# Performance work log

Hardware: AMD Instinct MI355X
Metric: run time of the kernel (lower is better)

Reference implementation:

```python
import jax, jax.numpy as jnp
import numpy as np

NX = 65536   # spatial cells
T = 32       # time points
H = 128      # MLP hidden width
DX = 1.0     # spatial resolution (init kwarg dx)
S0, S1 = -1.0, 1.0  # fixed stencil (learn_stencil=False)


def setup_inputs() -> dict:
    key = jax.random.key(0)
    k1, k2, k3, k4 = jax.random.split(key, 4)
    t = jnp.arange(T, dtype=jnp.float32) * 0.01          # time grid, dt=0.01
    u0 = jax.random.uniform(k1, (NX,), jnp.float32)      # initial state
    inv_sqrt_h = jnp.float32(1.0 / np.sqrt(H))
    W1 = jax.random.normal(k2, (1, H), jnp.float32)
    W2 = jax.random.normal(k3, (H, H), jnp.float32) * inv_sqrt_h
    W3 = jax.random.normal(k4, (H, 1), jnp.float32) * inv_sqrt_h
    D = jnp.full((1,), 0.01, jnp.float32)                # diffusion coefficient
    BC = jnp.zeros((2, 1), jnp.float32)                  # Dirichlet BC values
    return {"t": t, "u0": u0, "W1": W1, "W2": W2, "W3": W3, "D": D, "BC": BC}


def _flux(u, W1, W2, W3, D, BC):
    # per-cell MLP (func_nn): Linear->Tanh->Linear->Tanh->Linear, no bias, no sigmoid
    h = jnp.tanh(u[:, None] @ W1)        # [Nx, H]
    h = jnp.tanh(h @ W2)                 # [Nx, H]
    a = (h @ W3)[:, 0]                   # [Nx]
    a_plus = jax.nn.relu(a)
    a_min = -jax.nn.relu(-a)
    d = D[0]
    # left fluxes
    lb = d * (S0 * u[0] + S1 * BC[0, 0]) - a_plus[0] / DX * (-S0 * u[0] - S1 * BC[0, 0])
    ln = d * (S0 * u[1:] + S1 * u[:-1]) - a_plus[1:] / DX * (-S0 * u[1:] - S1 * u[:-1])
    left = jnp.concatenate([lb[None], ln])
    # right fluxes
    rb = d * (S0 * u[-1] + S1 * BC[1, 0]) - a_min[-1] / DX * (S0 * u[-1] + S1 * BC[1, 0])
    rn = d * (S0 * u[:-1] + S1 * u[1:]) - a_min[:-1] / DX * (S0 * u[:-1] + S1 * u[1:])
    right = jnp.concatenate([rn, rb[None]])
    return left + right


def reference(t, u0, W1, W2, W3, D, BC):
    # Neural-ODE integration of du/dt = flux_kernel(u); fixed-step RK4 over grid t
    f = lambda u: _flux(u, W1, W2, W3, D, BC)

    def step(u, dt):
        k1 = f(u)
        k2 = f(u + 0.5 * dt * k1)
        k3 = f(u + 0.5 * dt * k2)
        k4 = f(u + dt * k3)
        un = u + (dt / 6.0) * (k1 + 2.0 * k2 + 2.0 * k3 + k4)
        return un, un

    _, us = jax.lax.scan(step, u0, jnp.diff(t))
    return jnp.concatenate([u0[None], us], axis=0)  # [T, Nx]
```

## Files before the change

### kernel.cpp

```cpp
#include <hip/hip_runtime.h>

#define NXC 65536
#define TT 32
#define HH 128
#define TABN 6145
#define TABNP 6146
#define TABLO (-1.0f)
#define TABINV 2048.0f
#define OUTW 64
#define VC 3
#define WINW 192
#define HALO 64

typedef __attribute__((ext_vector_type(8))) short bf16x8;
typedef __attribute__((ext_vector_type(4))) float f32x4;
typedef unsigned short u16;

__device__ __forceinline__ float bf2f(u16 b) {
    union { unsigned int u; float f; } v; v.u = ((unsigned int)b) << 16; return v.f;
}
__device__ __forceinline__ u16 f2bf(float f) {
    union { float f; unsigned int u; } v; v.f = f;
    return (u16)((v.u + 0x7fffu + ((v.u >> 16) & 1u)) >> 16);
}
__device__ __forceinline__ bool is_bf16_mode(const void* t) {
    return ((const u16*)t)[1] != 0;
}

#if __has_builtin(__builtin_amdgcn_exp2f)
#define EXP2F(x) __builtin_amdgcn_exp2f(x)
#else
#define EXP2F(x) exp2f(x)
#endif
#if __has_builtin(__builtin_amdgcn_rcpf)
#define RCPF(x) __builtin_amdgcn_rcpf(x)
#else
#define RCPF(x) (1.0f / (x))
#endif
#if __has_builtin(__builtin_amdgcn_fractf)
#define FRACTF(x) __builtin_amdgcn_fractf(x)
#else
#define FRACTF(x) ((x) - floorf(x))
#endif

__device__ __forceinline__ float fast_tanh(float x) {
    float e = EXP2F(x * 2.8853900817779268f);
    return 1.0f - 2.0f * RCPF(e + 1.0f);
}

__device__ __forceinline__ float dpp_up1(float x) {
    int xi = __float_as_int(x);
    int r = __builtin_amdgcn_update_dpp(xi, xi, 0x138, 0xf, 0xf, false);
    return __int_as_float(r);
}
__device__ __forceinline__ float dpp_dn1(float x) {
    int xi = __float_as_int(x);
    int r = __builtin_amdgcn_update_dpp(xi, xi, 0x130, 0xf, 0xf, false);
    return __int_as_float(r);
}

__global__ void w2swz_kernel(const void* t, const void* W2,
                             u16* __restrict__ w2frag) {
    bool bf = is_bf16_mode(t);
    int i = blockIdx.x * 256 + threadIdx.x;
    int j = i & 7;
    int lane = (i >> 3) & 63;
    int ks = (i >> 9) & 3;
    int nt = i >> 11;
    int k = ks * 32 + (lane >> 4) * 8 + j;
    int n = nt * 16 + (lane & 15);
    w2frag[i] = bf ? ((const u16*)W2)[k * HH + n]
                   : f2bf(((const float*)W2)[k * HH + n]);
}

__global__ __launch_bounds__(256) void tabbuild_kernel(
    const void* traw, const void* W1, const void* W3,
    const u16* __restrict__ w2frag, float* __restrict__ atab) {
    __shared__ float w1s[HH];
    __shared__ float w3s[HH];
    bool bf = is_bf16_mode(traw);
    int tid = threadIdx.x;
    if (tid < HH)
        w1s[tid] = bf ? bf2f(((const u16*)W1)[tid]) : ((const float*)W1)[tid];
    else
        w3s[tid - HH] = bf ? bf2f(((const u16*)W3)[tid - HH])
                           : ((const float*)W3)[tid - HH];
    __syncthreads();

    int lane = tid & 63;
    int wave = tid >> 6;
    int q = lane >> 4;
    int m = lane & 15;
    int base = (blockIdx.x * 4 + wave) * 16;
    float uin = TABLO + (float)(base + m) * (1.0f / TABINV);

    bf16x8 afrag[4];
#pragma unroll
    for (int ks = 0; ks < 4; ++ks)
#pragma unroll
        for (int j = 0; j < 8; ++j) {
            float h = fast_tanh(uin * w1s[ks * 32 + q * 8 + j]);
            afrag[ks][j] = (short)f2bf(h);
        }

    const bf16x8* w2f = (const bf16x8*)w2frag;
    float p0 = 0.f, p1 = 0.f, p2 = 0.f, p3 = 0.f;
#pragma unroll
    for (int nt = 0; nt < 8; ++nt) {
        f32x4 acc = {0.f, 0.f, 0.f, 0.f};
#pragma unroll
        for (int ks = 0; ks < 4; ++ks) {
            bf16x8 b = w2f[(nt * 4 + ks) * 64 + lane];
            acc = __builtin_amdgcn_mfma_f32_16x16x32_bf16(afrag[ks], b, acc, 0, 0, 0);
        }
        float w3v = w3s[nt * 16 + m];
        p0 += fast_tanh(acc[0]) * w3v;
        p1 += fast_tanh(acc[1]) * w3v;
        p2 += fast_tanh(acc[2]) * w3v;
        p3 += fast_tanh(acc[3]) * w3v;
    }
#pragma unroll
    for (int sh = 1; sh < 16; sh <<= 1) {
        p0 += __shfl_xor(p0, sh, 64);
        p1 += __shfl_xor(p1, sh, 64);
        p2 += __shfl_xor(p2, sh, 64);
        p3 += __shfl_xor(p3, sh, 64);
    }
    int r = m & 3;
    float a = (r == 0) ? p0 : (r == 1) ? p1 : (r == 2) ? p2 : p3;
    if (m < 4) {
        int e = base + q * 4 + r;
        if (e < TABNP) atab[e] = a;
    }
}

__global__ __launch_bounds__(256) void chunk_kernel(
    const void* traw, const void* uin, float* __restrict__ uout,
    const void* Draw, const void* BCraw, const float* __restrict__ atab,
    void* __restrict__ outbase, int s0, int nsteps) {
    __shared__ __align__(16) float2 tab[TABN];
    __shared__ float t32s[TT];

    int tid = threadIdx.x;
    bool bf = is_bf16_mode(traw);

    for (int e = tid * 4; e < TABN - 1; e += 1024) {
        float4 qv = *(const float4*)(atab + e);
        float nx = atab[e + 4];
        float4 lo = make_float4(qv.x, qv.y - qv.x, qv.y, qv.z - qv.y);
        float4 hi = make_float4(qv.z, qv.w - qv.z, qv.w, nx - qv.w);
        *(float4*)(&tab[e]) = lo;
        *(float4*)(&tab[e + 2]) = hi;
    }
    if (tid == 0)
        tab[TABN - 1] = make_float2(atab[TABN - 1], atab[TABN] - atab[TABN - 1]);
    if (tid < TT)
        t32s[tid] = bf ? bf2f(((const u16*)traw)[tid]) : ((const float*)traw)[tid];

    float d   = bf ? bf2f(((const u16*)Draw)[0])  : ((const float*)Draw)[0];
    float bc0 = bf ? bf2f(((const u16*)BCraw)[0]) : ((const float*)BCraw)[0];
    float bc1 = bf ? bf2f(((const u16*)BCraw)[1]) : ((const float*)BCraw)[1];

    int lane = tid & 63;
    int wid = blockIdx.x * 4 + (tid >> 6);
    int gb = wid * OUTW - HALO + lane * VC;
    int i0 = lane * VC;
    bool first = (s0 == 0);
    bool edgeblk = (blockIdx.x == 0) || (blockIdx.x == gridDim.x - 1);

    float v[VC], ub[VC], gfix[VC];
    bool gok[VC], own[VC];
#pragma unroll
    for (int j = 0; j < VC; ++j) {
        int g = gb + j;
        int i = i0 + j;
        gok[j] = (g >= 0) && (g < NXC);
        own[j] = (i >= HALO) && (i < HALO + OUTW);
        float x;
        if (first) {
            if (bf) {
                u16 raw = gok[j] ? ((const u16*)uin)[g] : (u16)0;
                x = bf2f(raw);
                if (own[j]) ((u16*)outbase)[g] = raw;
            } else {
                float raw = gok[j] ? ((const float*)uin)[g] : 0.f;
                x = raw;
                if (own[j]) ((float*)outbase)[g] = raw;
            }
        } else {
            x = gok[j] ? ((const float*)uin)[g] : 0.f;
        }
        if (!gok[j]) x = (g < 0) ? bc0 : bc1;
        gfix[j] = x;
        v[j] = x;
        ub[j] = x;
    }
    __syncthreads();

    float pf[VC];
    float2 pt[VC];
#pragma unroll
    for (int j = 0; j < VC; ++j) {
        float f = fmaf(v[j], TABINV, (-TABLO) * TABINV);
        f = fminf(fmaxf(f, 0.0f), (float)(TABN - 1));
        int e0 = (int)f;
        pf[j] = FRACTF(f);
        pt[j] = tab[e0];
    }

    for (int st = 0; st < nsteps; ++st) {
        int step = s0 + st;
        float dt = t32s[step + 1] - t32s[step];
        float dt2 = 0.5f * dt, dt6 = dt * (1.0f / 6.0f);
        float kacc[VC], kv[VC];
#pragma unroll
        for (int j = 0; j < VC; ++j) kacc[j] = 0.f;
#pragma unroll
        for (int s = 0; s < 4; ++s) {
            float cnext = (s < 2) ? dt2 : dt;
            float wgt = (s == 1 || s == 2) ? 2.f : 1.f;
            float vup = dpp_up1(v[VC - 1]);
            float vdn = dpp_dn1(v[0]);
#pragma unroll
            for (int j = 0; j < VC; ++j) {
                float vc = v[j];
                float vl = (j == 0) ? vup : v[j - 1];
                float vr = (j == VC - 1) ? vdn : v[j + 1];
                float a = fmaf(pf[j], pt[j].y, pt[j].x);
                float ap = fmaxf(a, 0.f);
                float am = fminf(a, 0.f);
                kv[j] = (vl - vc) * (d + ap) + (vr - vc) * (d - am);
            }
#pragma unroll
            for (int j = 0; j < VC; ++j) {
                kacc[j] += wgt * kv[j];
                float nv = (s < 3) ? fmaf(cnext, kv[j], ub[j])
                                   : fmaf(dt6, kacc[j], ub[j]);
                v[j] = nv;
                if (s == 3) ub[j] = nv;
                float f = fmaf(v[j], TABINV, (-TABLO) * TABINV);
                f = fminf(fmaxf(f, 0.0f), (float)(TABN - 1));
                int e0 = (int)f;
                pf[j] = FRACTF(f);
                pt[j] = tab[e0];
            }
            if (edgeblk) {
#pragma unroll
                for (int j = 0; j < VC; ++j)
                    if (!gok[j]) { v[j] = gfix[j]; ub[j] = gfix[j]; }
            }
        }
        if (bf) {
            u16* orow = (u16*)outbase + (size_t)(step + 1) * NXC;
#pragma unroll
            for (int j = 0; j < VC; ++j)
                if (own[j]) orow[gb + j] = f2bf(ub[j]);
        } else {
            float* orow = (float*)outbase + (size_t)(step + 1) * NXC;
#pragma unroll
            for (int j = 0; j < VC; ++j)
                if (own[j]) orow[gb + j] = ub[j];
        }
    }
    if (uout != nullptr) {
#pragma unroll
        for (int j = 0; j < VC; ++j)
            if (own[j]) uout[gb + j] = ub[j];
    }
}

extern "C" void kernel_launch(void* const* d_in, const int* in_sizes, int n_in,
                              void* d_out, int out_size, void* d_ws,
                              size_t ws_size, hipStream_t stream) {
    const void* t  = d_in[0];
    const void* u0 = d_in[1];
    const void* W1 = d_in[2];
    const void* W2 = d_in[3];
    const void* W3 = d_in[4];
    const void* Dp = d_in[5];
    const void* BC = d_in[6];

    float* atab = (float*)d_ws;
    u16* w2frag = (u16*)(atab + TABNP + 2);
    float* uB = (float*)(w2frag + 16384);

    w2swz_kernel<<<64, 256, 0, stream>>>(t, W2, w2frag);
    tabbuild_kernel<<<(TABNP + 63) / 64, 256, 0, stream>>>(t, W1, W3, w2frag, atab);

    chunk_kernel<<<NXC / (OUTW * 4), 256, 0, stream>>>(t, u0, uB, Dp, BC, atab,
                                                       d_out, 0, 16);
    chunk_kernel<<<NXC / (OUTW * 4), 256, 0, stream>>>(t, uB, nullptr, Dp, BC, atab,
                                                       d_out, 16, 15);
}
```

Measured before the change: 98.23 us.

## Process two interleaved 32-cell windows per wave with a wider halo

Each wave now integrates two independent 192-cell windows. Each window owns 32 output cells and carries an 80-cell halo, where before a single window owned 64 outputs with a 64-cell halo. The launch grid stays the same size, so each thread holds twice the state. The two independent dependency chains are meant to give instruction-level parallelism that hides the LDS table-lookup and DPP latency at the low wave occupancy of one block per CU. The cost is twice as much redundant halo computation per output cell, plus more registers.

```diff
diff --git a/kernel.cpp b/kernel.cpp
--- a/kernel.cpp
+++ b/kernel.cpp
@@ -7,10 +7,11 @@
 #define TABNP 6146
 #define TABLO (-1.0f)
 #define TABINV 2048.0f
-#define OUTW 64
+#define OUTW 32
 #define VC 3
 #define WINW 192
-#define HALO 64
+#define HALO 80
+#define NW 2
 
 typedef __attribute__((ext_vector_type(8))) short bf16x8;
 typedef __attribute__((ext_vector_type(4))) float f32x4;
@@ -163,109 +164,136 @@
 
     int lane = tid & 63;
     int wid = blockIdx.x * 4 + (tid >> 6);
-    int gb = wid * OUTW - HALO + lane * VC;
     int i0 = lane * VC;
     bool first = (s0 == 0);
     bool edgeblk = (blockIdx.x == 0) || (blockIdx.x == gridDim.x - 1);
 
-    float v[VC], ub[VC], gfix[VC];
-    bool gok[VC], own[VC];
+    int gbw[NW];
+    float v[NW][VC], ub[NW][VC], gfix[NW][VC];
+    bool gok[NW][VC], own[VC];
 #pragma unroll
     for (int j = 0; j < VC; ++j) {
-        int g = gb + j;
         int i = i0 + j;
-        gok[j] = (g >= 0) && (g < NXC);
         own[j] = (i >= HALO) && (i < HALO + OUTW);
-        float x;
-        if (first) {
-            if (bf) {
-                u16 raw = gok[j] ? ((const u16*)uin)[g] : (u16)0;
-                x = bf2f(raw);
-                if (own[j]) ((u16*)outbase)[g] = raw;
+    }
+#pragma unroll
+    for (int w = 0; w < NW; ++w) {
+        gbw[w] = (wid * NW + w) * OUTW - HALO + i0;
+#pragma unroll
+        for (int j = 0; j < VC; ++j) {
+            int g = gbw[w] + j;
+            gok[w][j] = (g >= 0) && (g < NXC);
+            float x;
+            if (first) {
+                if (bf) {
+                    u16 raw = gok[w][j] ? ((const u16*)uin)[g] : (u16)0;
+                    x = bf2f(raw);
+                    if (own[j]) ((u16*)outbase)[g] = raw;
+                } else {
+                    float raw = gok[w][j] ? ((const float*)uin)[g] : 0.f;
+                    x = raw;
+                    if (own[j]) ((float*)outbase)[g] = raw;
+                }
             } else {
-                float raw = gok[j] ? ((const float*)uin)[g] : 0.f;
-                x = raw;
-                if (own[j]) ((float*)outbase)[g] = raw;
+                x = gok[w][j] ? ((const float*)uin)[g] : 0.f;
             }
-        } else {
-            x = gok[j] ? ((const float*)uin)[g] : 0.f;
-        }
-        if (!gok[j]) x = (g < 0) ? bc0 : bc1;
-        gfix[j] = x;
-        v[j] = x;
-        ub[j] = x;
+            if (!gok[w][j]) x = (g < 0) ? bc0 : bc1;
+            gfix[w][j] = x;
+            v[w][j] = x;
+            ub[w][j] = x;
+        }
     }
     __syncthreads();
 
-    float pf[VC];
-    float2 pt[VC];
-#pragma unroll
-    for (int j = 0; j < VC; ++j) {
-        float f = fmaf(v[j], TABINV, (-TABLO) * TABINV);
-        f = fminf(fmaxf(f, 0.0f), (float)(TABN - 1));
-        int e0 = (int)f;
-        pf[j] = FRACTF(f);
-        pt[j] = tab[e0];
-    }
+    float pf[NW][VC];
+    float2 pt[NW][VC];
+#pragma unroll
+    for (int w = 0; w < NW; ++w)
+#pragma unroll
+        for (int j = 0; j < VC; ++j) {
+            float f = fmaf(v[w][j], TABINV, (-TABLO) * TABINV);
+            f = fminf(fmaxf(f, 0.0f), (float)(TABN - 1));
+            int e0 = (int)f;
+            pf[w][j] = FRACTF(f);
+            pt[w][j] = tab[e0];
+        }
 
     for (int st = 0; st < nsteps; ++st) {
         int step = s0 + st;
         float dt = t32s[step + 1] - t32s[step];
         float dt2 = 0.5f * dt, dt6 = dt * (1.0f / 6.0f);
-        float kacc[VC], kv[VC];
-#pragma unroll
-        for (int j = 0; j < VC; ++j) kacc[j] = 0.f;
+        float kacc[NW][VC], kv[NW][VC];
+#pragma unroll
+        for (int w = 0; w < NW; ++w)
+#pragma unroll
+            for (int j = 0; j < VC; ++j) kacc[w][j] = 0.f;
 #pragma unroll
         for (int s = 0; s < 4; ++s) {
             float cnext = (s < 2) ? dt2 : dt;
             float wgt = (s == 1 || s == 2) ? 2.f : 1.f;
-            float vup = dpp_up1(v[VC - 1]);
-            float vdn = dpp_dn1(v[0]);
-#pragma unroll
-            for (int j = 0; j < VC; ++j) {
-                float vc = v[j];
-                float vl = (j == 0) ? vup : v[j - 1];
-                float vr = (j == VC - 1) ? vdn : v[j + 1];
-                float a = fmaf(pf[j], pt[j].y, pt[j].x);
-                float ap = fmaxf(a, 0.f);
-                float am = fminf(a, 0.f);
-                kv[j] = (vl - vc) * (d + ap) + (vr - vc) * (d - am);
+            float vup[NW], vdn[NW];
+#pragma unroll
+            for (int w = 0; w < NW; ++w) {
+                vup[w] = dpp_up1(v[w][VC - 1]);
+                vdn[w] = dpp_dn1(v[w][0]);
             }
 #pragma unroll
-            for (int j = 0; j < VC; ++j) {
-                kacc[j] += wgt * kv[j];
-                float nv = (s < 3) ? fmaf(cnext, kv[j], ub[j])
-                                   : fmaf(dt6, kacc[j], ub[j]);
-                v[j] = nv;
-                if (s == 3) ub[j] = nv;
-                float f = fmaf(v[j], TABINV, (-TABLO) * TABINV);
-                f = fminf(fmaxf(f, 0.0f), (float)(TABN - 1));
-                int e0 = (int)f;
-                pf[j] = FRACTF(f);
-                pt[j] = tab[e0];
-            }
+            for (int w = 0; w < NW; ++w)
+#pragma unroll
+                for (int j = 0; j < VC; ++j) {
+                    float vc = v[w][j];
+                    float vl = (j == 0) ? vup[w] : v[w][j - 1];
+                    float vr = (j == VC - 1) ? vdn[w] : v[w][j + 1];
+                    float a = fmaf(pf[w][j], pt[w][j].y, pt[w][j].x);
+                    float ap = fmaxf(a, 0.f);
+                    float am = fminf(a, 0.f);
+                    kv[w][j] = (vl - vc) * (d + ap) + (vr - vc) * (d - am);
+                }
+#pragma unroll
+            for (int w = 0; w < NW; ++w)
+#pragma unroll
+                for (int j = 0; j < VC; ++j) {
+                    kacc[w][j] += wgt * kv[w][j];
+                    float nv = (s < 3) ? fmaf(cnext, kv[w][j], ub[w][j])
+                                       : fmaf(dt6, kacc[w][j], ub[w][j]);
+                    v[w][j] = nv;
+                    if (s == 3) ub[w][j] = nv;
+                    float f = fmaf(v[w][j], TABINV, (-TABLO) * TABINV);
+                    f = fminf(fmaxf(f, 0.0f), (float)(TABN - 1));
+                    int e0 = (int)f;
+                    pf[w][j] = FRACTF(f);
+                    pt[w][j] = tab[e0];
+                }
             if (edgeblk) {
 #pragma unroll
-                for (int j = 0; j < VC; ++j)
-                    if (!gok[j]) { v[j] = gfix[j]; ub[j] = gfix[j]; }
+                for (int w = 0; w < NW; ++w)
+#pragma unroll
+                    for (int j = 0; j < VC; ++j)
+                        if (!gok[w][j]) { v[w][j] = gfix[w][j]; ub[w][j] = gfix[w][j]; }
             }
         }
         if (bf) {
             u16* orow = (u16*)outbase + (size_t)(step + 1) * NXC;
 #pragma unroll
-            for (int j = 0; j < VC; ++j)
-                if (own[j]) orow[gb + j] = f2bf(ub[j]);
+            for (int w = 0; w < NW; ++w)
+#pragma unroll
+                for (int j = 0; j < VC; ++j)
+                    if (own[j]) orow[gbw[w] + j] = f2bf(ub[w][j]);
         } else {
             float* orow = (float*)outbase + (size_t)(step + 1) * NXC;
 #pragma unroll
+            for (int w = 0; w < NW; ++w)
+#pragma unroll
+                for (int j = 0; j < VC; ++j)
+                    if (own[j]) orow[gbw[w] + j] = ub[w][j];
+        }
+    }
+    if (uout != nullptr) {
+#pragma unroll
+        for (int w = 0; w < NW; ++w)
+#pragma unroll
             for (int j = 0; j < VC; ++j)
-                if (own[j]) orow[gb + j] = ub[j];
-        }
-    }
-    if (uout != nullptr) {
-#pragma unroll
-        for (int j = 0; j < VC; ++j)
-            if (own[j]) uout[gb + j] = ub[j];
+                if (own[j]) uout[gbw[w] + j] = ub[w][j];
     }
 }
 
@@ -287,8 +315,7 @@
     w2swz_kernel<<<64, 256, 0, stream>>>(t, W2, w2frag);
     tabbuild_kernel<<<(TABNP + 63) / 64, 256, 0, stream>>>(t, W1, W3, w2frag, atab);
 
-    chunk_kernel<<<NXC / (OUTW * 4), 256, 0, stream>>>(t, u0, uB, Dp, BC, atab,
-                                                       d_out, 0, 16);
-    chunk_kernel<<<NXC / (OUTW * 4), 256, 0, stream>>>(t, uB, nullptr, Dp, BC, atab,
-                                                       d_out, 16, 15);
-}
+    const int grid = NXC / (OUTW * NW * 4);
+    chunk_kernel<<<grid, 256, 0, stream>>>(t, u0, uB, Dp, BC, atab, d_out, 0, 16);
+    chunk_kernel<<<grid, 256, 0, stream>>>(t, uB, nullptr, Dp, BC, atab, d_out, 16, 15);
+}
```

Measured after the change: 114.5 us. +16.6%, slower.
